# Kernel tuning notes

Measured on AMD Instinct MI355X. Metric: run time of the kernel, lower is better.

The kernel has to match this reference:

```python
import jax, jax.numpy as jnp
import numpy as np

SIGMA_MAX = 0.3
GAMMA = 1.0
COV_SHRINK = 0.1
COV_DELTA = 1e-3
BN_EPS = 1e-5
PATCH = 3


def setup_inputs() -> dict:
    key = jax.random.key(0)
    ks = jax.random.split(key, 5)
    B, K, C, H, W = 2, 8, 64, 128, 128
    X = jax.random.normal(ks[0], (B, K, C, H, W), dtype=jnp.float32)
    w1 = jax.random.normal(ks[1], (C // 2, C), dtype=jnp.float32) * 0.1
    w2 = jax.random.normal(ks[2], (1, C // 2), dtype=jnp.float32) * 0.1
    return {
        "X": X,
        "w1": w1,
        "bn_scale": jnp.ones((C // 2,), jnp.float32),
        "bn_bias": jnp.zeros((C // 2,), jnp.float32),
        "bn_mean": jnp.zeros((C // 2,), jnp.float32),
        "bn_var": jnp.ones((C // 2,), jnp.float32),
        "w2": w2,
        "a0_raw": jax.random.normal(ks[3], (K,), dtype=jnp.float32) * 0.1,
        "sigma_raw": jax.random.normal(ks[4], (K,), dtype=jnp.float32) * 0.1,
    }


def _forward(X, w1, bn_scale, bn_bias, bn_mean, bn_var, w2, a0_raw, sigma_raw):
    B, K, C, H, W = X.shape
    # --- SensorMapGenerator: 1x1 conv -> BN (inference) -> ReLU -> 1x1 conv ---
    Xf = X.reshape(B * K, C, H, W)
    h = jnp.einsum('oc,bchw->bohw', w1, Xf)                       # [BK, C/2, H, W]
    inv_std = bn_scale / jnp.sqrt(bn_var + BN_EPS)
    h = h * inv_std[None, :, None, None] + (bn_bias - bn_mean * inv_std)[None, :, None, None]
    h = jax.nn.relu(h)
    S = jnp.einsum('oc,bchw->bohw', w2, h).reshape(B, K, H, W)    # scalar sensor maps

    # --- CovarianceEstimator: reflect pad, 3x3 patches, center, R = PP^T/N ---
    pad = PATCH // 2
    Sp = jnp.pad(S, ((0, 0), (0, 0), (pad, pad), (pad, pad)), mode='reflect')
    patches = jnp.stack(
        [Sp[:, :, i:i + H, j:j + W] for i in range(PATCH) for j in range(PATCH)],
        axis=-1)                                                  # [B, K, H, W, N]
    N = PATCH * PATCH
    patches = patches.transpose(0, 2, 3, 1, 4)                    # [B, H, W, K, N]
    pc = patches - patches.mean(axis=-1, keepdims=True)
    R = jnp.matmul(pc, pc.swapaxes(-1, -2)) / N                   # [B, H, W, K, K]

    # --- Guidance vector and uncertainty (stage mode) ---
    a0 = jax.nn.softmax(a0_raw)                                   # [K], sums to 1
    sigma = SIGMA_MAX * jax.nn.sigmoid(sigma_raw)                 # [K]

    # --- Robust diagonal-loaded Capon solve per pixel ---
    # R_reg = (1-shrink)*R + shrink*(tr R / K)*I + delta*I + gamma*diag(sigma^2)
    I = jnp.eye(K, dtype=R.dtype)
    tr = jnp.trace(R, axis1=-2, axis2=-1)                         # [B, H, W]
    load = COV_DELTA * I + GAMMA * jnp.diag(sigma * sigma)
    R_load = (1.0 - COV_SHRINK) * R + (COV_SHRINK * tr / K)[..., None, None] * I + load
    rhs = jnp.broadcast_to(a0[:, None], R_load.shape[:-2] + (K, 1))
    w_un = jnp.linalg.solve(R_load, rhs)[..., 0]                  # [B, H, W, K]
    denom = jnp.einsum('bhwk,k->bhw', w_un, a0)
    w = w_un / denom[..., None]                                   # a0^T w = 1

    # --- Weighted fusion over streams ---
    Y = jnp.einsum('bhwk,bkchw->bchw', w, X)                      # [B, C, H, W]
    return Y


def reference(X, w1, bn_scale, bn_bias, bn_mean, bn_var, w2, a0_raw, sigma_raw):
    return _forward(X, w1, bn_scale, bn_bias, bn_mean, bn_var, w2, a0_raw, sigma_raw)
```

## Files before the change

### kernel.cpp

```cpp
#include <hip/hip_runtime.h>
#include <hip/hip_bf16.h>
#include <math.h>

#define B_    2
#define K_    8
#define C_    64
#define CH_   32
#define H_    128
#define W_    128
#define HW_   16384
#define BN_EPS 1e-5f
#define SIGMA_MAX 0.3f
#define COV_SHRINK 0.1f
#define COV_DELTA 1e-3f

__global__ void prep_kernel(const float* __restrict__ w1,
                            const float* __restrict__ bn_scale,
                            const float* __restrict__ bn_bias,
                            const float* __restrict__ bn_mean,
                            const float* __restrict__ bn_var,
                            const float* __restrict__ w2,
                            const float* __restrict__ a0_raw,
                            const float* __restrict__ sigma_raw,
                            float* __restrict__ par) {
    int t = threadIdx.x;
    for (int i = t; i < CH_ * C_; i += blockDim.x) {
        int c = i >> 5;
        int o = i & 31;
        float inv = bn_scale[o] / sqrtf(bn_var[o] + BN_EPS);
        par[c * CH_ + o] = w1[o * C_ + c] * inv;
    }
    if (t < CH_) {
        float inv = bn_scale[t] / sqrtf(bn_var[t] + BN_EPS);
        par[2048 + t] = bn_bias[t] - bn_mean[t] * inv;
        par[2080 + t] = w2[t];
    }
    if (t < K_) {
        float m = -1e30f;
        for (int i = 0; i < K_; ++i) m = fmaxf(m, a0_raw[i]);
        float s = 0.f;
        for (int i = 0; i < K_; ++i) s += expf(a0_raw[i] - m);
        par[2112 + t] = expf(a0_raw[t] - m) / s;
        float sg = SIGMA_MAX / (1.f + expf(-sigma_raw[t]));
        par[2120 + t] = sg * sg;
    }
}

__global__ void __launch_bounds__(256)
stage1_kernel(const float* __restrict__ X,
              const float* __restrict__ wf,
              const float* __restrict__ beff,
              const float* __restrict__ w2,
              float* __restrict__ S) {
    int idx = blockIdx.x * blockDim.x + threadIdx.x;
    int hw = idx & (HW_ - 1);
    int bk = idx >> 14;
    const float* xp = X + (size_t)bk * (C_ * HW_) + hw;

    float acc[CH_];
#pragma unroll
    for (int o = 0; o < CH_; ++o) acc[o] = beff[o];

#pragma unroll 4
    for (int c = 0; c < C_; ++c) {
        float xv = xp[(size_t)c * HW_];
        const float* wrow = wf + c * CH_;
#pragma unroll
        for (int o = 0; o < CH_; ++o) acc[o] = fmaf(wrow[o], xv, acc[o]);
    }
    float s = 0.f;
#pragma unroll
    for (int o = 0; o < CH_; ++o) s = fmaf(w2[o], fmaxf(acc[o], 0.f), s);
    S[idx] = s;
}

__global__ void capon_kernel(const float* __restrict__ S,
                             const float* __restrict__ a0,
                             const float* __restrict__ sig2,
                             float* __restrict__ wOut) {
    int idx = blockIdx.x * blockDim.x + threadIdx.x;
    int b  = idx >> 14;
    int hw = idx & (HW_ - 1);
    int h  = hw >> 7;
    int w  = hw & (W_ - 1);

    int hm = (h == 0)      ? 1       : h - 1;
    int hp = (h == H_ - 1) ? H_ - 2  : h + 1;
    int wm = (w == 0)      ? 1       : w - 1;
    int wp = (w == W_ - 1) ? W_ - 2  : w + 1;
    int row0 = hm * W_, row1 = h * W_, row2 = hp * W_;
    int rows[3] = {row0, row1, row2};
    int cols[3] = {wm, w, wp};

    float pc[K_][9];
#pragma unroll
    for (int k = 0; k < K_; ++k) {
        const float* sp = S + (((size_t)b * K_ + k) << 14);
        float p[9];
        float m = 0.f;
#pragma unroll
        for (int i = 0; i < 3; ++i)
#pragma unroll
            for (int j = 0; j < 3; ++j) {
                float v = sp[rows[i] + cols[j]];
                p[i * 3 + j] = v;
                m += v;
            }
        m *= (1.f / 9.f);
#pragma unroll
        for (int n = 0; n < 9; ++n) pc[k][n] = p[n] - m;
    }

    float A[K_][K_];
    float tr = 0.f;
#pragma unroll
    for (int i = 0; i < K_; ++i) {
        float s = 0.f;
#pragma unroll
        for (int n = 0; n < 9; ++n) s = fmaf(pc[i][n], pc[i][n], s);
        s *= (1.f / 9.f);
        tr += s;
        A[i][i] = s;
    }
#pragma unroll
    for (int i = 0; i < K_; ++i)
#pragma unroll
        for (int j = 0; j < i; ++j) {
            float s = 0.f;
#pragma unroll
            for (int n = 0; n < 9; ++n) s = fmaf(pc[i][n], pc[j][n], s);
            A[i][j] = (1.f - COV_SHRINK) * s * (1.f / 9.f);
        }
    float dl = COV_SHRINK * tr * (1.f / (float)K_) + COV_DELTA;
#pragma unroll
    for (int i = 0; i < K_; ++i)
        A[i][i] = (1.f - COV_SHRINK) * A[i][i] + dl + sig2[i];

#pragma unroll
    for (int j = 0; j < K_; ++j) {
        float d = A[j][j];
#pragma unroll
        for (int t = 0; t < j; ++t) d = fmaf(-A[j][t], A[j][t], d);
        d = sqrtf(d);
        A[j][j] = d;
        float inv = 1.f / d;
#pragma unroll
        for (int i = j + 1; i < K_; ++i) {
            float s = A[i][j];
#pragma unroll
            for (int t = 0; t < j; ++t) s = fmaf(-A[i][t], A[j][t], s);
            A[i][j] = s * inv;
        }
    }
    float z[K_];
#pragma unroll
    for (int i = 0; i < K_; ++i) {
        float s = a0[i];
#pragma unroll
        for (int t = 0; t < i; ++t) s = fmaf(-A[i][t], z[t], s);
        z[i] = s / A[i][i];
    }
    float x[K_];
#pragma unroll
    for (int i = K_ - 1; i >= 0; --i) {
        float s = z[i];
#pragma unroll
        for (int t = i + 1; t < K_; ++t) s = fmaf(-A[t][i], x[t], s);
        x[i] = s / A[i][i];
    }
    float denom = 0.f;
#pragma unroll
    for (int k = 0; k < K_; ++k) denom = fmaf(x[k], a0[k], denom);
    float invd = 1.f / denom;

    float4 o0 = make_float4(x[0] * invd, x[1] * invd, x[2] * invd, x[3] * invd);
    float4 o1 = make_float4(x[4] * invd, x[5] * invd, x[6] * invd, x[7] * invd);
    float4* dst = (float4*)(wOut + (size_t)idx * K_);
    dst[0] = o0;
    dst[1] = o1;
}

__global__ void __launch_bounds__(256)
fuse_kernel(const float* __restrict__ X,
            const float* __restrict__ wW,
            float* __restrict__ out) {
    int idx = blockIdx.x * blockDim.x + threadIdx.x;
    int hw = idx & (HW_ - 1);
    int bc = idx >> 14;
    int b = bc >> 6;
    int c = bc & (C_ - 1);
    size_t pix = ((size_t)b << 14) + hw;

    const float4* wv4 = (const float4*)(wW + pix * K_);
    float4 wa = wv4[0];
    float4 wb = wv4[1];

    const float* xp = X + (((size_t)b * K_) * C_ + c) * HW_ + hw;
    const size_t kstride = (size_t)C_ * HW_;

    float acc;
    acc = wa.x * xp[0];
    acc = fmaf(wa.y, xp[kstride * 1], acc);
    acc = fmaf(wa.z, xp[kstride * 2], acc);
    acc = fmaf(wa.w, xp[kstride * 3], acc);
    acc = fmaf(wb.x, xp[kstride * 4], acc);
    acc = fmaf(wb.y, xp[kstride * 5], acc);
    acc = fmaf(wb.z, xp[kstride * 6], acc);
    acc = fmaf(wb.w, xp[kstride * 7], acc);
    out[idx] = acc;
}

extern "C" void kernel_launch(void* const* d_in, const int* in_sizes, int n_in,
                              void* d_out, int out_size, void* d_ws, size_t ws_size,
                              hipStream_t stream) {
    const float* X         = (const float*)d_in[0];
    const float* w1        = (const float*)d_in[1];
    const float* bn_scale  = (const float*)d_in[2];
    const float* bn_bias   = (const float*)d_in[3];
    const float* bn_mean   = (const float*)d_in[4];
    const float* bn_var    = (const float*)d_in[5];
    const float* w2        = (const float*)d_in[6];
    const float* a0_raw    = (const float*)d_in[7];
    const float* sigma_raw = (const float*)d_in[8];
    float* out = (float*)d_out;
    float* ws  = (float*)d_ws;

    float* par = ws;
    float* S   = ws + 4096;
    float* wW  = ws + 4096 + (B_ * K_ * HW_);

    prep_kernel<<<1, 256, 0, stream>>>(w1, bn_scale, bn_bias, bn_mean, bn_var,
                                       w2, a0_raw, sigma_raw, par);

    int n1 = B_ * K_ * HW_;
    stage1_kernel<<<n1 / 256, 256, 0, stream>>>(X, par, par + 2048, par + 2080, S);

    int n2 = B_ * HW_;
    capon_kernel<<<n2 / 256, 256, 0, stream>>>(S, par + 2112, par + 2120, wW);

    int n3 = B_ * C_ * HW_;
    fuse_kernel<<<n3 / 256, 256, 0, stream>>>(X, wW, out);
}
```

Baseline: 136.9 us.

## Fuse Capon solve with stream fusion and process two pixels per stage1 thread

Result: slower. 159.0 us (+16.1%).

```diff
diff --git a/kernel.cpp b/kernel.cpp
--- a/kernel.cpp
+++ b/kernel.cpp
@@ -1,5 +1,4 @@
 #include <hip/hip_runtime.h>
-#include <hip/hip_bf16.h>
 #include <math.h>
 
 #define B_    2
@@ -13,6 +12,8 @@
 #define SIGMA_MAX 0.3f
 #define COV_SHRINK 0.1f
 #define COV_DELTA 1e-3f
+
+#define TILE_ 64
 
 __global__ void prep_kernel(const float* __restrict__ w1,
                             const float* __restrict__ bn_scale,
@@ -53,161 +54,173 @@
               const float* __restrict__ w2,
               float* __restrict__ S) {
     int idx = blockIdx.x * blockDim.x + threadIdx.x;
-    int hw = idx & (HW_ - 1);
-    int bk = idx >> 14;
-    const float* xp = X + (size_t)bk * (C_ * HW_) + hw;
-
-    float acc[CH_];
-#pragma unroll
-    for (int o = 0; o < CH_; ++o) acc[o] = beff[o];
+    int hw2 = idx & (HW_ / 2 - 1);
+    int bk  = idx >> 13;
+    const float* xp = X + (size_t)bk * (C_ * HW_) + (size_t)hw2 * 2;
+
+    float a0c[CH_], a1c[CH_];
+#pragma unroll
+    for (int o = 0; o < CH_; ++o) {
+        float b = beff[o];
+        a0c[o] = b;
+        a1c[o] = b;
+    }
 
 #pragma unroll 4
     for (int c = 0; c < C_; ++c) {
-        float xv = xp[(size_t)c * HW_];
+        float2 xv = *(const float2*)(xp + (size_t)c * HW_);
         const float* wrow = wf + c * CH_;
 #pragma unroll
-        for (int o = 0; o < CH_; ++o) acc[o] = fmaf(wrow[o], xv, acc[o]);
-    }
-    float s = 0.f;
-#pragma unroll
-    for (int o = 0; o < CH_; ++o) s = fmaf(w2[o], fmaxf(acc[o], 0.f), s);
-    S[idx] = s;
-}
-
-__global__ void capon_kernel(const float* __restrict__ S,
-                             const float* __restrict__ a0,
-                             const float* __restrict__ sig2,
-                             float* __restrict__ wOut) {
-    int idx = blockIdx.x * blockDim.x + threadIdx.x;
-    int b  = idx >> 14;
-    int hw = idx & (HW_ - 1);
-    int h  = hw >> 7;
-    int w  = hw & (W_ - 1);
-
-    int hm = (h == 0)      ? 1       : h - 1;
-    int hp = (h == H_ - 1) ? H_ - 2  : h + 1;
-    int wm = (w == 0)      ? 1       : w - 1;
-    int wp = (w == W_ - 1) ? W_ - 2  : w + 1;
-    int row0 = hm * W_, row1 = h * W_, row2 = hp * W_;
-    int rows[3] = {row0, row1, row2};
-    int cols[3] = {wm, w, wp};
-
-    float pc[K_][9];
-#pragma unroll
-    for (int k = 0; k < K_; ++k) {
-        const float* sp = S + (((size_t)b * K_ + k) << 14);
-        float p[9];
-        float m = 0.f;
-#pragma unroll
-        for (int i = 0; i < 3; ++i)
-#pragma unroll
-            for (int j = 0; j < 3; ++j) {
-                float v = sp[rows[i] + cols[j]];
-                p[i * 3 + j] = v;
-                m += v;
+        for (int o = 0; o < CH_; ++o) {
+            float wv = wrow[o];
+            a0c[o] = fmaf(wv, xv.x, a0c[o]);
+            a1c[o] = fmaf(wv, xv.y, a1c[o]);
+        }
+    }
+    float s0 = 0.f, s1 = 0.f;
+#pragma unroll
+    for (int o = 0; o < CH_; ++o) {
+        float wv = w2[o];
+        s0 = fmaf(wv, fmaxf(a0c[o], 0.f), s0);
+        s1 = fmaf(wv, fmaxf(a1c[o], 0.f), s1);
+    }
+    *(float2*)(S + (size_t)idx * 2) = make_float2(s0, s1);
+}
+
+__global__ void __launch_bounds__(256)
+capon_fuse_kernel(const float* __restrict__ X,
+                  const float* __restrict__ S,
+                  const float* __restrict__ a0,
+                  const float* __restrict__ sig2,
+                  float* __restrict__ out) {
+    __shared__ float wL[TILE_][K_ + 1];
+
+    int tid   = threadIdx.x;
+    int gbase = blockIdx.x * TILE_;
+    int b      = gbase >> 14;
+    int hwbase = gbase & (HW_ - 1);
+
+    if (tid < TILE_) {
+        int hw = hwbase + tid;
+        int h  = hw >> 7;
+        int w  = hw & (W_ - 1);
+
+        int hm = (h == 0)      ? 1      : h - 1;
+        int hp = (h == H_ - 1) ? H_ - 2 : h + 1;
+        int wm = (w == 0)      ? 1      : w - 1;
+        int wp = (w == W_ - 1) ? W_ - 2 : w + 1;
+        int rows[3] = {hm * W_, h * W_, hp * W_};
+        int cols[3] = {wm, w, wp};
+
+        float pc[K_][9];
+#pragma unroll
+        for (int k = 0; k < K_; ++k) {
+            const float* sp = S + (((size_t)b * K_ + k) << 14);
+            float p[9];
+            float m = 0.f;
+#pragma unroll
+            for (int i = 0; i < 3; ++i)
+#pragma unroll
+                for (int j = 0; j < 3; ++j) {
+                    float v = sp[rows[i] + cols[j]];
+                    p[i * 3 + j] = v;
+                    m += v;
+                }
+            m *= (1.f / 9.f);
+#pragma unroll
+            for (int n = 0; n < 9; ++n) pc[k][n] = p[n] - m;
+        }
+
+        float A[K_][K_];
+        float tr = 0.f;
+#pragma unroll
+        for (int i = 0; i < K_; ++i) {
+            float s = 0.f;
+#pragma unroll
+            for (int n = 0; n < 9; ++n) s = fmaf(pc[i][n], pc[i][n], s);
+            s *= (1.f / 9.f);
+            tr += s;
+            A[i][i] = s;
+        }
+#pragma unroll
+        for (int i = 0; i < K_; ++i)
+#pragma unroll
+            for (int j = 0; j < i; ++j) {
+                float s = 0.f;
+#pragma unroll
+                for (int n = 0; n < 9; ++n) s = fmaf(pc[i][n], pc[j][n], s);
+                A[i][j] = (1.f - COV_SHRINK) * s * (1.f / 9.f);
             }
-        m *= (1.f / 9.f);
-#pragma unroll
-        for (int n = 0; n < 9; ++n) pc[k][n] = p[n] - m;
-    }
-
-    float A[K_][K_];
-    float tr = 0.f;
-#pragma unroll
-    for (int i = 0; i < K_; ++i) {
-        float s = 0.f;
-#pragma unroll
-        for (int n = 0; n < 9; ++n) s = fmaf(pc[i][n], pc[i][n], s);
-        s *= (1.f / 9.f);
-        tr += s;
-        A[i][i] = s;
-    }
-#pragma unroll
-    for (int i = 0; i < K_; ++i)
-#pragma unroll
-        for (int j = 0; j < i; ++j) {
-            float s = 0.f;
-#pragma unroll
-            for (int n = 0; n < 9; ++n) s = fmaf(pc[i][n], pc[j][n], s);
-            A[i][j] = (1.f - COV_SHRINK) * s * (1.f / 9.f);
-        }
-    float dl = COV_SHRINK * tr * (1.f / (float)K_) + COV_DELTA;
-#pragma unroll
-    for (int i = 0; i < K_; ++i)
-        A[i][i] = (1.f - COV_SHRINK) * A[i][i] + dl + sig2[i];
-
-#pragma unroll
-    for (int j = 0; j < K_; ++j) {
-        float d = A[j][j];
-#pragma unroll
-        for (int t = 0; t < j; ++t) d = fmaf(-A[j][t], A[j][t], d);
-        d = sqrtf(d);
-        A[j][j] = d;
-        float inv = 1.f / d;
-#pragma unroll
-        for (int i = j + 1; i < K_; ++i) {
-            float s = A[i][j];
-#pragma unroll
-            for (int t = 0; t < j; ++t) s = fmaf(-A[i][t], A[j][t], s);
-            A[i][j] = s * inv;
-        }
-    }
-    float z[K_];
-#pragma unroll
-    for (int i = 0; i < K_; ++i) {
-        float s = a0[i];
-#pragma unroll
-        for (int t = 0; t < i; ++t) s = fmaf(-A[i][t], z[t], s);
-        z[i] = s / A[i][i];
-    }
-    float x[K_];
-#pragma unroll
-    for (int i = K_ - 1; i >= 0; --i) {
-        float s = z[i];
-#pragma unroll
-        for (int t = i + 1; t < K_; ++t) s = fmaf(-A[t][i], x[t], s);
-        x[i] = s / A[i][i];
-    }
-    float denom = 0.f;
-#pragma unroll
-    for (int k = 0; k < K_; ++k) denom = fmaf(x[k], a0[k], denom);
-    float invd = 1.f / denom;
-
-    float4 o0 = make_float4(x[0] * invd, x[1] * invd, x[2] * invd, x[3] * invd);
-    float4 o1 = make_float4(x[4] * invd, x[5] * invd, x[6] * invd, x[7] * invd);
-    float4* dst = (float4*)(wOut + (size_t)idx * K_);
-    dst[0] = o0;
-    dst[1] = o1;
-}
-
-__global__ void __launch_bounds__(256)
-fuse_kernel(const float* __restrict__ X,
-            const float* __restrict__ wW,
-            float* __restrict__ out) {
-    int idx = blockIdx.x * blockDim.x + threadIdx.x;
-    int hw = idx & (HW_ - 1);
-    int bc = idx >> 14;
-    int b = bc >> 6;
-    int c = bc & (C_ - 1);
-    size_t pix = ((size_t)b << 14) + hw;
-
-    const float4* wv4 = (const float4*)(wW + pix * K_);
-    float4 wa = wv4[0];
-    float4 wb = wv4[1];
-
-    const float* xp = X + (((size_t)b * K_) * C_ + c) * HW_ + hw;
+        float dl = COV_SHRINK * tr * (1.f / (float)K_) + COV_DELTA;
+#pragma unroll
+        for (int i = 0; i < K_; ++i)
+            A[i][i] = (1.f - COV_SHRINK) * A[i][i] + dl + sig2[i];
+
+#pragma unroll
+        for (int j = 0; j < K_; ++j) {
+            float d = A[j][j];
+#pragma unroll
+            for (int t = 0; t < j; ++t) d = fmaf(-A[j][t], A[j][t], d);
+            d = sqrtf(d);
+            A[j][j] = d;
+            float inv = 1.f / d;
+#pragma unroll
+            for (int i = j + 1; i < K_; ++i) {
+                float s = A[i][j];
+#pragma unroll
+                for (int t = 0; t < j; ++t) s = fmaf(-A[i][t], A[j][t], s);
+                A[i][j] = s * inv;
+            }
+        }
+        float z[K_];
+#pragma unroll
+        for (int i = 0; i < K_; ++i) {
+            float s = a0[i];
+#pragma unroll
+            for (int t = 0; t < i; ++t) s = fmaf(-A[i][t], z[t], s);
+            z[i] = s / A[i][i];
+        }
+        float x[K_];
+#pragma unroll
+        for (int i = K_ - 1; i >= 0; --i) {
+            float s = z[i];
+#pragma unroll
+            for (int t = i + 1; t < K_; ++t) s = fmaf(-A[t][i], x[t], s);
+            x[i] = s / A[i][i];
+        }
+        float denom = 0.f;
+#pragma unroll
+        for (int k = 0; k < K_; ++k) denom = fmaf(x[k], a0[k], denom);
+        float invd = 1.f / denom;
+#pragma unroll
+        for (int k = 0; k < K_; ++k) wL[tid][k] = x[k] * invd;
+    }
+    __syncthreads();
+
+    int px = tid & (TILE_ - 1);
+    int c4 = tid >> 6;
+    float wr[K_];
+#pragma unroll
+    for (int k = 0; k < K_; ++k) wr[k] = wL[px][k];
+
+    const float* xb = X + ((size_t)b * K_ * C_) * HW_ + hwbase + px;
+    float* ob = out + ((size_t)b * C_) * HW_ + hwbase + px;
     const size_t kstride = (size_t)C_ * HW_;
 
-    float acc;
-    acc = wa.x * xp[0];
-    acc = fmaf(wa.y, xp[kstride * 1], acc);
-    acc = fmaf(wa.z, xp[kstride * 2], acc);
-    acc = fmaf(wa.w, xp[kstride * 3], acc);
-    acc = fmaf(wb.x, xp[kstride * 4], acc);
-    acc = fmaf(wb.y, xp[kstride * 5], acc);
-    acc = fmaf(wb.z, xp[kstride * 6], acc);
-    acc = fmaf(wb.w, xp[kstride * 7], acc);
-    out[idx] = acc;
+#pragma unroll 4
+    for (int cc = 0; cc < C_ / 4; ++cc) {
+        int c = (cc << 2) | c4;
+        const float* xp = xb + (size_t)c * HW_;
+        float acc = wr[0] * xp[0];
+        acc = fmaf(wr[1], xp[kstride * 1], acc);
+        acc = fmaf(wr[2], xp[kstride * 2], acc);
+        acc = fmaf(wr[3], xp[kstride * 3], acc);
+        acc = fmaf(wr[4], xp[kstride * 4], acc);
+        acc = fmaf(wr[5], xp[kstride * 5], acc);
+        acc = fmaf(wr[6], xp[kstride * 6], acc);
+        acc = fmaf(wr[7], xp[kstride * 7], acc);
+        ob[(size_t)c * HW_] = acc;
+    }
 }
 
 extern "C" void kernel_launch(void* const* d_in, const int* in_sizes, int n_in,
@@ -227,17 +240,13 @@
 
     float* par = ws;
     float* S   = ws + 4096;
-    float* wW  = ws + 4096 + (B_ * K_ * HW_);
 
     prep_kernel<<<1, 256, 0, stream>>>(w1, bn_scale, bn_bias, bn_mean, bn_var,
                                        w2, a0_raw, sigma_raw, par);
 
-    int n1 = B_ * K_ * HW_;
+    int n1 = B_ * K_ * HW_ / 2;
     stage1_kernel<<<n1 / 256, 256, 0, stream>>>(X, par, par + 2048, par + 2080, S);
 
-    int n2 = B_ * HW_;
-    capon_kernel<<<n2 / 256, 256, 0, stream>>>(S, par + 2112, par + 2120, wW);
-
-    int n3 = B_ * C_ * HW_;
-    fuse_kernel<<<n3 / 256, 256, 0, stream>>>(X, wW, out);
-}
+    int n2 = B_ * HW_ / TILE_;
+    capon_fuse_kernel<<<n2, 256, 0, stream>>>(X, S, par + 2112, par + 2120, out);
+}
```
